# Kernel tuning notes

Hardware: AMD Instinct MI355X
Metric: run time of the kernel (lower is better)

The kernel has to match this reference:

```python
import jax, jax.numpy as jnp
import numpy as np
from jax import lax

OBS_LEN = 8
PRED_LEN = 12
BATCH = 131072
EMB = 128
HID = 128


def _lstm_cell(h, c, x, Wih, Whh, b):
    # PyTorch LSTM gate order: i, f, g, o
    z = x @ Wih + h @ Whh + b  # (B, 4H)
    i, f, g, o = jnp.split(z, 4, axis=-1)
    c_new = jax.nn.sigmoid(f) * c + jax.nn.sigmoid(i) * jnp.tanh(g)
    h_new = jax.nn.sigmoid(o) * jnp.tanh(c_new)
    return h_new, c_new


def setup_inputs() -> dict:
    key = jax.random.key(0)
    ks = jax.random.split(key, 8)
    p = lambda k, s: jax.random.normal(k, s, dtype=jnp.float32) * 0.1
    return {
        "obs_traj": jax.random.normal(ks[0], (OBS_LEN, BATCH, 2), dtype=jnp.float32),
        # encoder input embedding (Linear 2 -> EMB)
        "We": p(ks[1], (2, EMB)), "be": jnp.zeros((EMB,), jnp.float32),
        # encoder LSTM
        "Wih_e": p(ks[2], (EMB, 4 * HID)), "Whh_e": p(ks[3], (HID, 4 * HID)),
        "b_e": jnp.zeros((4 * HID,), jnp.float32),
        # decoder input embedding (Linear 2 -> EMB)
        "Wd": p(ks[4], (2, EMB)), "bd": jnp.zeros((EMB,), jnp.float32),
        # decoder LSTM
        "Wih_d": p(ks[5], (EMB, 4 * HID)), "Whh_d": p(ks[6], (HID, 4 * HID)),
        "b_d": jnp.zeros((4 * HID,), jnp.float32),
        # hidden2pos (Linear HID -> 2)
        "Wo": p(ks[7], (HID, 2)), "bo": jnp.zeros((2,), jnp.float32),
        "pred_len": PRED_LEN,
    }


def reference(obs_traj, We, be, Wih_e, Whh_e, b_e, Wd, bd, Wih_d, Whh_d, b_d, Wo, bo, pred_len):
    B = obs_traj.shape[1]
    H = Whh_e.shape[0]
    dt = obs_traj.dtype

    # ---- Encoder: embed positions, run LSTM over obs_len ----
    emb = obs_traj @ We + be  # (obs_len, B, EMB)
    h0 = jnp.zeros((B, H), dt)
    c0 = jnp.zeros((B, H), dt)

    def enc_step(carry, x_t):
        h, c = carry
        h, c = _lstm_cell(h, c, x_t, Wih_e, Whh_e, b_e)
        return (h, c), None

    (h_enc, _), _ = lax.scan(enc_step, (h0, c0), emb)

    # ---- Decoder: state = (h_final, zeros); first pos directly from h_final ----
    pos0 = h_enc @ Wo + bo  # (B, 2)
    h_d = h_enc
    c_d = jnp.zeros_like(h_enc)

    def dec_step(carry, _):
        h, c, pos = carry
        x = pos @ Wd + bd  # embed previous predicted position
        h, c = _lstm_cell(h, c, x, Wih_d, Whh_d, b_d)
        pos_new = h @ Wo + bo
        return (h, c, pos_new), pos_new

    _, rest = lax.scan(dec_step, (h_d, c_d, pos0), None, length=pred_len - 1)
    pred_traj = jnp.concatenate([pos0[None], rest], axis=0)  # (pred_len, B, 2)
    return pred_traj
```

## Files before the change

### kernel.cpp

```cpp
#include <hip/hip_runtime.h>


#define OBS_LEN 8
#define PRED_LEN 12
#define BATCH 131072
#define HID 128
#define NZ 512
#define KWT 128
#define XK 32
#define A2S 40

typedef float f32x4 __attribute__((ext_vector_type(4)));
typedef float f32x2 __attribute__((ext_vector_type(2)));
typedef unsigned short u16x8 __attribute__((ext_vector_type(8)));
typedef __bf16 bf16x8 __attribute__((ext_vector_type(8)));

#define K2F 1.4426950408889634f

static __device__ __forceinline__ unsigned short cvt1(float f) {
  __bf16 b = (__bf16)f;
  return __builtin_bit_cast(unsigned short, b);
}
static __device__ __forceinline__ float bf2f(unsigned short h) {
  return __uint_as_float(((unsigned int)h) << 16);
}

__global__ void prep_weights(const float* __restrict__ We,   const float* __restrict__ be,
                             const float* __restrict__ Wih_e,const float* __restrict__ Whh_e,
                             const float* __restrict__ b_e,
                             const float* __restrict__ Wd,   const float* __restrict__ bd,
                             const float* __restrict__ Wih_d,const float* __restrict__ Whh_d,
                             const float* __restrict__ b_d,
                             const float* __restrict__ Wo,   const float* __restrict__ bo,
                             unsigned short* __restrict__ wt_enc,
                             unsigned short* __restrict__ wt_dec,
                             unsigned short* __restrict__ xw_enc,
                             float* __restrict__ auxf_dec) {
  const int c = blockIdx.x & (NZ - 1);
  const bool dec = blockIdx.x >= NZ;
  const int cg = c >> 6, gate = (c >> 4) & 3, cl = c & 15;
  const int unit = cg * 16 + cl;
  const int n = gate * HID + unit;
  const float s = (gate == 2) ? (-2.f * K2F) : (-K2F);

  const float* Whh = dec ? Whh_d : Whh_e;
  const float* Wih = dec ? Wih_d : Wih_e;
  const float* Wem = dec ? Wd : We;
  const float* bem = dec ? bd : be;
  const float* bl  = dec ? b_d : b_e;
  unsigned short* wt = dec ? wt_dec : wt_enc;

  float wx = 0.f, wy = 0.f;
  for (int e = 0; e < HID; ++e) {
    wx += Wem[e] * Wih[e * NZ + n];
    wy += Wem[HID + e] * Wih[e * NZ + n];
  }
  for (int k = threadIdx.x; k < KWT; k += 64) {
    float v = Whh[k * NZ + n];
    if (dec) v += Wo[k * 2] * wx + Wo[k * 2 + 1] * wy;
    wt[c * KWT + k] = cvt1(s * v);
  }
  if (threadIdx.x == 0) {
    float bb = bl[n];
    for (int e = 0; e < HID; ++e) bb += bem[e] * Wih[e * NZ + n];
    if (dec) {
      bb += bo[0] * wx + bo[1] * wy;
      auxf_dec[c] = s * bb;
    } else {
      unsigned short* xr = xw_enc + c * XK;
      for (int k = 5; k < XK; ++k) xr[k] = 0;
      xr[0] = cvt1(s * wx); xr[1] = cvt1(s * wy); xr[2] = cvt1(s * bb);
      xr[3] = xr[0]; xr[4] = xr[1];
    }
  }
}


#define MFMA(A, B, C)                                                          \
  __builtin_amdgcn_mfma_f32_16x16x32_bf16(                                     \
      __builtin_bit_cast(bf16x8, (A)), __builtin_bit_cast(bf16x8, (B)), (C),   \
      0, 0, 0)

#define EXP4(D, S)                                                             \
  { f32x4 _s = (S);                                                            \
    D[0] = __builtin_amdgcn_exp2f(_s[0]); D[1] = __builtin_amdgcn_exp2f(_s[1]);\
    D[2] = __builtin_amdgcn_exp2f(_s[2]); D[3] = __builtin_amdgcn_exp2f(_s[3]); }
#define RCP4(D, S)                                                             \
  { f32x4 _r = (S);                                                            \
    D[0] = __builtin_amdgcn_rcpf(_r[0]); D[1] = __builtin_amdgcn_rcpf(_r[1]);  \
    D[2] = __builtin_amdgcn_rcpf(_r[2]); D[3] = __builtin_amdgcn_rcpf(_r[3]); }

#define LOADW_BF(WT)                                                           \
  { _Pragma("unroll")                                                          \
    for (int kc = 0; kc < 4; ++kc) {                                           \
      _Pragma("unroll")                                                        \
      for (int g = 0; g < 4; ++g)                                              \
        bfr[kc][g] =                                                           \
            *(const u16x8*)&(WT)[(cg * 64 + g * 16 + l15) * KWT + kc * 32 +    \
                                 l4 * 8];                                      \
    } }

#define MMH(ACC, X)                                                            \
  { _Pragma("unroll")                                                          \
    for (int kc = 0; kc < 4; ++kc) {                                           \
      const int mm_g = (((kc * 4 + l4) ^ l15) << 3);                           \
      u16x8 mm_a0 = *(const u16x8*)&hL[(X)*4096 + l15 * 128 + mm_g];           \
      u16x8 mm_a1 = *(const u16x8*)&hL[(X)*4096 + (16 + l15) * 128 + mm_g];    \
      _Pragma("unroll")                                                        \
      for (int g = 0; g < 4; ++g) {                                            \
        ACC[0][g] = MFMA(mm_a0, bfr[kc][g], ACC[0][g]);                        \
        ACC[1][g] = MFMA(mm_a1, bfr[kc][g], ACC[1][g]);                        \
      } } }

#define MMXE(ACC, X)                                                           \
  { u16x8 mm_a2a = *(const u16x8*)&A2[(X)*32 * A2S + l15 * A2S + l4 * 8];      \
    u16x8 mm_a2b =                                                             \
        *(const u16x8*)&A2[(X)*32 * A2S + (16 + l15) * A2S + l4 * 8];          \
    _Pragma("unroll")                                                          \
    for (int g = 0; g < 4; ++g) {                                              \
      ACC[0][g] = MFMA(mm_a2a, xfr[g], ZROV);                                  \
      ACC[1][g] = MFMA(mm_a2b, xfr[g], ZROV);                                  \
    }                                                                          \
    MMH(ACC, X) }

#define INITD(ACC)                                                             \
  { _Pragma("unroll")                                                          \
    for (int m = 0; m < 2; ++m) {                                              \
      _Pragma("unroll")                                                        \
      for (int g = 0; g < 4; ++g)                                              \
        ACC[m][g] = (f32x4){bbD[g], bbD[g], bbD[g], bbD[g]};                   \
    } }

#define GATEC(ACC, CRR, X)                                                     \
  { _Pragma("unroll")                                                          \
    for (int m = 0; m < 2; ++m) {                                              \
      f32x4 g_eB, g_eA, g_eG, g_eO;                                            \
      EXP4(g_eB, ACC[m][0]) EXP4(g_eA, ACC[m][1])                              \
      EXP4(g_eG, ACC[m][2]) EXP4(g_eO, ACC[m][3])                              \
      f32x4 g_a1 = 1.f + g_eA, g_b1 = 1.f + g_eB, g_g1 = 1.f + g_eG;           \
      f32x4 g_bg = g_b1 * g_g1;                                                \
      f32x4 g_rd; RCP4(g_rd, g_a1 * g_bg)                                      \
      f32x4 g_cv = (CRR[m] * g_bg + (1.f - g_eG) * g_a1) * g_rd;               \
      CRR[m] = g_cv;                                                           \
      f32x4 g_eC; EXP4(g_eC, g_cv * (-2.f * K2F))                              \
      f32x4 g_rh; RCP4(g_rh, (1.f + g_eO) * (1.f + g_eC))                      \
      f32x4 g_hv = (1.f - g_eC) * g_rh;                                        \
      const int g_R0 = 16 * m + l4 * 4;                                        \
      _Pragma("unroll")                                                        \
      for (int r = 0; r < 4; ++r)                                              \
        hL[(X)*4096 + (g_R0 + r) * 128 +                                       \
           ((uh ^ ((g_R0 + r) & 15)) << 3) + ul] = cvt1(g_hv[r]);              \
    } }

#define POSC(S, X)                                                             \
  { const int pp_r = tid >> 4;                                                 \
    u16x8 pp_h = *(const u16x8*)&hL[(X)*4096 + pp_r * 128 +                    \
                                    ((pq ^ (pp_r & 15)) << 3)];                \
    f32x2 pp_s = (f32x2){0.f, 0.f};                                            \
    pp_s += bf2f(pp_h[0]) * (f32x2){wo0[0], wo0[1]};                           \
    pp_s += bf2f(pp_h[1]) * (f32x2){wo0[2], wo0[3]};                           \
    pp_s += bf2f(pp_h[2]) * (f32x2){wo1[0], wo1[1]};                           \
    pp_s += bf2f(pp_h[3]) * (f32x2){wo1[2], wo1[3]};                           \
    pp_s += bf2f(pp_h[4]) * (f32x2){wo2[0], wo2[1]};                           \
    pp_s += bf2f(pp_h[5]) * (f32x2){wo2[2], wo2[3]};                           \
    pp_s += bf2f(pp_h[6]) * (f32x2){wo3[0], wo3[1]};                           \
    pp_s += bf2f(pp_h[7]) * (f32x2){wo3[2], wo3[3]};                           \
    pp_s[0] += __shfl_xor(pp_s[0], 1); pp_s[1] += __shfl_xor(pp_s[1], 1);      \
    pp_s[0] += __shfl_xor(pp_s[0], 2); pp_s[1] += __shfl_xor(pp_s[1], 2);      \
    pp_s[0] += __shfl_xor(pp_s[0], 4); pp_s[1] += __shfl_xor(pp_s[1], 4);      \
    pp_s[0] += __shfl_xor(pp_s[0], 8); pp_s[1] += __shfl_xor(pp_s[1], 8);      \
    if (pq == 0) {                                                             \
      float2 pp_o; pp_o.x = pp_s[0] + bo0; pp_o.y = pp_s[1] + bo1;             \
      ((float2*)out)[(size_t)(S)*BATCH + row0 + (X)*32 + pp_r] = pp_o;         \
    } }

#define STAGE_OBS_A2(T, X)                                                     \
  if (tid < 32) {                                                              \
    float2 so_p =                                                              \
        ((const float2*)obs)[(size_t)(T)*BATCH + row0 + (X)*32 + tid];         \
    unsigned short so_x = cvt1(so_p.x), so_y = cvt1(so_p.y);                   \
    unsigned short* so_r = &A2[(X)*32 * A2S + tid * A2S];                      \
    so_r[0] = so_x; so_r[1] = so_y; so_r[2] = 0x3F80u;                         \
    so_r[3] = cvt1(so_p.x - bf2f(so_x));                                       \
    so_r[4] = cvt1(so_p.y - bf2f(so_y));                                       \
  }

__global__ __launch_bounds__(512, 2) void lstm_fused(
    const float* __restrict__ obs,
    const unsigned short* __restrict__ wt_enc,
    const unsigned short* __restrict__ wt_dec,
    const unsigned short* __restrict__ xw_enc,
    const float* __restrict__ auxf_dec,
    const float* __restrict__ Wo, const float* __restrict__ bo,
    float* __restrict__ out) {
  __shared__ unsigned short hL[2 * 32 * 128];
  __shared__ unsigned short A2[2 * 32 * A2S];

  const int tid = threadIdx.x;
  const int lane = tid & 63;
  const int cg = tid >> 6;
  const int l15 = lane & 15;
  const int l4 = lane >> 4;
  const int pq = tid & 15;
  const int row0 = blockIdx.x * 64;
  const int u = cg * 16 + l15, uh = u >> 3, ul = u & 7;
  const float bo0 = bo[0], bo1 = bo[1];
  const f32x4 ZROV = {0.f, 0.f, 0.f, 0.f};

  {
    u16x8 z8 = (u16x8){0, 0, 0, 0, 0, 0, 0, 0};
    *(u16x8*)&hL[tid * 8] = z8;
    *(u16x8*)&hL[4096 + tid * 8] = z8;
    unsigned short* az = &A2[tid * 5];
    az[0] = 0; az[1] = 0; az[2] = 0; az[3] = 0; az[4] = 0;
  }
  const float* wop = Wo + pq * 16;
  const f32x4 wo0 = *(const f32x4*)wop;
  const f32x4 wo1 = *(const f32x4*)(wop + 4);
  const f32x4 wo2 = *(const f32x4*)(wop + 8);
  const f32x4 wo3 = *(const f32x4*)(wop + 12);

  u16x8 bfr[4][4], xfr[4];
  LOADW_BF(wt_enc);
#pragma unroll
  for (int g = 0; g < 4; ++g)
    xfr[g] = *(const u16x8*)&xw_enc[(cg * 64 + g * 16 + l15) * XK + l4 * 8];

  f32x4 accA[2][4], accB[2][4];
  f32x4 crrA[2], crrB[2];
  crrA[0] = crrA[1] = ZROV;
  crrB[0] = crrB[1] = ZROV;
  __syncthreads();

  STAGE_OBS_A2(0, 0)
  __syncthreads();

#pragma unroll 1
  for (int t = 0; t < OBS_LEN; ++t) {
    if (t > 0) { GATEC(accB, crrB, 1) }
    STAGE_OBS_A2(t, 1)
    MMXE(accA, 0)
    __syncthreads();
    GATEC(accA, crrA, 0)
    if (t + 1 < OBS_LEN) { STAGE_OBS_A2(t + 1, 0) }
    MMXE(accB, 1)
    __syncthreads();
  }

  LOADW_BF(wt_dec);
  float bbD[4];
#pragma unroll
  for (int g = 0; g < 4; ++g) bbD[g] = auxf_dec[cg * 64 + g * 16 + l15];
  crrA[0] = crrA[1] = ZROV;

  GATEC(accB, crrB, 1)
  POSC(0, 0)
  INITD(accA)
  MMH(accA, 0)
  __syncthreads();
  crrB[0] = crrB[1] = ZROV;

  GATEC(accA, crrA, 0)
  POSC(0, 1)
  INITD(accB)
  MMH(accB, 1)
  __syncthreads();

#pragma unroll 1
  for (int d = 2; d < PRED_LEN; ++d) {
    GATEC(accB, crrB, 1)
    POSC(d - 1, 0)
    INITD(accA)
    MMH(accA, 0)
    __syncthreads();
    GATEC(accA, crrA, 0)
    POSC(d - 1, 1)
    INITD(accB)
    MMH(accB, 1)
    __syncthreads();
  }

  GATEC(accB, crrB, 1)
  POSC(PRED_LEN - 1, 0)
  __syncthreads();
  POSC(PRED_LEN - 1, 1)
}

extern "C" void kernel_launch(void* const* d_in, const int* in_sizes, int n_in,
                              void* d_out, int out_size, void* d_ws, size_t ws_size,
                              hipStream_t stream) {
  const float* obs   = (const float*)d_in[0];
  const float* We    = (const float*)d_in[1];
  const float* be    = (const float*)d_in[2];
  const float* Wih_e = (const float*)d_in[3];
  const float* Whh_e = (const float*)d_in[4];
  const float* b_e   = (const float*)d_in[5];
  const float* Wd    = (const float*)d_in[6];
  const float* bd    = (const float*)d_in[7];
  const float* Wih_d = (const float*)d_in[8];
  const float* Whh_d = (const float*)d_in[9];
  const float* b_d   = (const float*)d_in[10];
  const float* Wo    = (const float*)d_in[11];
  const float* bo    = (const float*)d_in[12];
  float* out = (float*)d_out;

  unsigned short* wt_enc = (unsigned short*)d_ws;
  unsigned short* wt_dec = wt_enc + NZ * KWT;
  unsigned short* xw_enc = wt_dec + NZ * KWT;
  float* auxf_dec = (float*)(xw_enc + NZ * XK);

  hipLaunchKernelGGL(prep_weights, dim3(2 * NZ), dim3(64), 0, stream,
                     We, be, Wih_e, Whh_e, b_e, Wd, bd, Wih_d, Whh_d, b_d,
                     Wo, bo, wt_enc, wt_dec, xw_enc, auxf_dec);
  hipLaunchKernelGGL(lstm_fused, dim3(BATCH / 64), dim3(512), 0, stream,
                     obs, wt_enc, wt_dec, xw_enc, auxf_dec, Wo, bo, out);
}
```

Measured before the change: 502.2 us.

## Double-buffer LSTM hidden state to halve barriers per timestep

Ping-pong buffers for the hidden state in LDS and for the staged observation inputs let both 32-row halves run their matmuls, then both gate updates, with a single barrier per timestep instead of two. The old schedule staggered the two halves to overlap gate math with MFMA. The new one groups all MFMAs and then all gate math inside each step. The decoder bias is also folded into the first MFMA's accumulator input instead of being set with separate initialisation. LDS use doubles, which may limit occupancy, and the interleaving of the two halves across barriers is lost.

```diff
diff --git a/kernel.cpp b/kernel.cpp
--- a/kernel.cpp
+++ b/kernel.cpp
@@ -9,6 +9,7 @@
 #define KWT 128
 #define XK 32
 #define A2S 40
+#define A2Q (2 * 32 * A2S)
 
 typedef float f32x4 __attribute__((ext_vector_type(4)));
 typedef float f32x2 __attribute__((ext_vector_type(2)));
@@ -100,38 +101,54 @@
                                  l4 * 8];                                      \
     } }
 
-#define MMH(ACC, X)                                                            \
+#define MMH(ACC, X, P)                                                         \
   { _Pragma("unroll")                                                          \
     for (int kc = 0; kc < 4; ++kc) {                                           \
       const int mm_g = (((kc * 4 + l4) ^ l15) << 3);                           \
-      u16x8 mm_a0 = *(const u16x8*)&hL[(X)*4096 + l15 * 128 + mm_g];           \
-      u16x8 mm_a1 = *(const u16x8*)&hL[(X)*4096 + (16 + l15) * 128 + mm_g];    \
+      const int mb = (X)*8192 + (P)*4096;                                      \
+      u16x8 mm_a0 = *(const u16x8*)&hL[mb + l15 * 128 + mm_g];                 \
+      u16x8 mm_a1 = *(const u16x8*)&hL[mb + (16 + l15) * 128 + mm_g];          \
       _Pragma("unroll")                                                        \
       for (int g = 0; g < 4; ++g) {                                            \
         ACC[0][g] = MFMA(mm_a0, bfr[kc][g], ACC[0][g]);                        \
         ACC[1][g] = MFMA(mm_a1, bfr[kc][g], ACC[1][g]);                        \
       } } }
 
-#define MMXE(ACC, X)                                                           \
-  { u16x8 mm_a2a = *(const u16x8*)&A2[(X)*32 * A2S + l15 * A2S + l4 * 8];      \
+#define MMXE(ACC, X, P, Q)                                                     \
+  { u16x8 mm_a2a =                                                             \
+        *(const u16x8*)&A2[(Q)*A2Q + ((X)*32 + l15) * A2S + l4 * 8];           \
     u16x8 mm_a2b =                                                             \
-        *(const u16x8*)&A2[(X)*32 * A2S + (16 + l15) * A2S + l4 * 8];          \
+        *(const u16x8*)&A2[(Q)*A2Q + ((X)*32 + 16 + l15) * A2S + l4 * 8];      \
     _Pragma("unroll")                                                          \
     for (int g = 0; g < 4; ++g) {                                              \
       ACC[0][g] = MFMA(mm_a2a, xfr[g], ZROV);                                  \
       ACC[1][g] = MFMA(mm_a2b, xfr[g], ZROV);                                  \
     }                                                                          \
-    MMH(ACC, X) }
-
-#define INITD(ACC)                                                             \
-  { _Pragma("unroll")                                                          \
-    for (int m = 0; m < 2; ++m) {                                              \
-      _Pragma("unroll")                                                        \
-      for (int g = 0; g < 4; ++g)                                              \
-        ACC[m][g] = (f32x4){bbD[g], bbD[g], bbD[g], bbD[g]};                   \
-    } }
-
-#define GATEC(ACC, CRR, X)                                                     \
+    MMH(ACC, X, P) }
+
+#define MMHD(ACC, X, P)                                                        \
+  { { const int mm_g = ((l4 ^ l15) << 3);                                      \
+      const int mb = (X)*8192 + (P)*4096;                                      \
+      u16x8 mm_a0 = *(const u16x8*)&hL[mb + l15 * 128 + mm_g];                 \
+      u16x8 mm_a1 = *(const u16x8*)&hL[mb + (16 + l15) * 128 + mm_g];          \
+      _Pragma("unroll")                                                        \
+      for (int g = 0; g < 4; ++g) {                                            \
+        ACC[0][g] = MFMA(mm_a0, bfr[0][g], bbV[g]);                            \
+        ACC[1][g] = MFMA(mm_a1, bfr[0][g], bbV[g]);                            \
+      } }                                                                      \
+    _Pragma("unroll")                                                          \
+    for (int kc = 1; kc < 4; ++kc) {                                           \
+      const int mm_g = (((kc * 4 + l4) ^ l15) << 3);                           \
+      const int mb = (X)*8192 + (P)*4096;                                      \
+      u16x8 mm_a0 = *(const u16x8*)&hL[mb + l15 * 128 + mm_g];                 \
+      u16x8 mm_a1 = *(const u16x8*)&hL[mb + (16 + l15) * 128 + mm_g];          \
+      _Pragma("unroll")                                                        \
+      for (int g = 0; g < 4; ++g) {                                            \
+        ACC[0][g] = MFMA(mm_a0, bfr[kc][g], ACC[0][g]);                        \
+        ACC[1][g] = MFMA(mm_a1, bfr[kc][g], ACC[1][g]);                        \
+      } } }
+
+#define GATEC(ACC, CRR, X, P)                                                  \
   { _Pragma("unroll")                                                          \
     for (int m = 0; m < 2; ++m) {                                              \
       f32x4 g_eB, g_eA, g_eG, g_eO;                                            \
@@ -148,13 +165,13 @@
       const int g_R0 = 16 * m + l4 * 4;                                        \
       _Pragma("unroll")                                                        \
       for (int r = 0; r < 4; ++r)                                              \
-        hL[(X)*4096 + (g_R0 + r) * 128 +                                       \
+        hL[(X)*8192 + (P)*4096 + (g_R0 + r) * 128 +                            \
            ((uh ^ ((g_R0 + r) & 15)) << 3) + ul] = cvt1(g_hv[r]);              \
     } }
 
-#define POSC(S, X)                                                             \
+#define POSC(S, X, P)                                                          \
   { const int pp_r = tid >> 4;                                                 \
-    u16x8 pp_h = *(const u16x8*)&hL[(X)*4096 + pp_r * 128 +                    \
+    u16x8 pp_h = *(const u16x8*)&hL[(X)*8192 + (P)*4096 + pp_r * 128 +         \
                                     ((pq ^ (pp_r & 15)) << 3)];                \
     f32x2 pp_s = (f32x2){0.f, 0.f};                                            \
     pp_s += bf2f(pp_h[0]) * (f32x2){wo0[0], wo0[1]};                           \
@@ -174,12 +191,11 @@
       ((float2*)out)[(size_t)(S)*BATCH + row0 + (X)*32 + pp_r] = pp_o;         \
     } }
 
-#define STAGE_OBS_A2(T, X)                                                     \
-  if (tid < 32) {                                                              \
-    float2 so_p =                                                              \
-        ((const float2*)obs)[(size_t)(T)*BATCH + row0 + (X)*32 + tid];         \
+#define STAGE_A2(T, Q)                                                         \
+  if (tid < 64) {                                                              \
+    float2 so_p = ((const float2*)obs)[(size_t)(T)*BATCH + row0 + tid];        \
     unsigned short so_x = cvt1(so_p.x), so_y = cvt1(so_p.y);                   \
-    unsigned short* so_r = &A2[(X)*32 * A2S + tid * A2S];                      \
+    unsigned short* so_r = &A2[(Q)*A2Q + tid * A2S];                           \
     so_r[0] = so_x; so_r[1] = so_y; so_r[2] = 0x3F80u;                         \
     so_r[3] = cvt1(so_p.x - bf2f(so_x));                                       \
     so_r[4] = cvt1(so_p.y - bf2f(so_y));                                       \
@@ -193,8 +209,8 @@
     const float* __restrict__ auxf_dec,
     const float* __restrict__ Wo, const float* __restrict__ bo,
     float* __restrict__ out) {
-  __shared__ unsigned short hL[2 * 32 * 128];
-  __shared__ unsigned short A2[2 * 32 * A2S];
+  __shared__ unsigned short hL[2 * 2 * 32 * 128];
+  __shared__ unsigned short A2[2 * A2Q];
 
   const int tid = threadIdx.x;
   const int lane = tid & 63;
@@ -210,9 +226,10 @@
   {
     u16x8 z8 = (u16x8){0, 0, 0, 0, 0, 0, 0, 0};
     *(u16x8*)&hL[tid * 8] = z8;
-    *(u16x8*)&hL[4096 + tid * 8] = z8;
-    unsigned short* az = &A2[tid * 5];
+    *(u16x8*)&hL[8192 + tid * 8] = z8;
+    unsigned short* az = &A2[tid * 10];
     az[0] = 0; az[1] = 0; az[2] = 0; az[3] = 0; az[4] = 0;
+    az[5] = 0; az[6] = 0; az[7] = 0; az[8] = 0; az[9] = 0;
   }
   const float* wop = Wo + pq * 16;
   const f32x4 wo0 = *(const f32x4*)wop;
@@ -232,58 +249,44 @@
   crrB[0] = crrB[1] = ZROV;
   __syncthreads();
 
-  STAGE_OBS_A2(0, 0)
+  STAGE_A2(0, 0)
   __syncthreads();
 
 #pragma unroll 1
   for (int t = 0; t < OBS_LEN; ++t) {
-    if (t > 0) { GATEC(accB, crrB, 1) }
-    STAGE_OBS_A2(t, 1)
-    MMXE(accA, 0)
+    const int p = t & 1;
+    if (t + 1 < OBS_LEN) { STAGE_A2(t + 1, p ^ 1) }
+    MMXE(accA, 0, p, p)
+    MMXE(accB, 1, p, p)
+    GATEC(accA, crrA, 0, p ^ 1)
+    GATEC(accB, crrB, 1, p ^ 1)
     __syncthreads();
-    GATEC(accA, crrA, 0)
-    if (t + 1 < OBS_LEN) { STAGE_OBS_A2(t + 1, 0) }
-    MMXE(accB, 1)
+  }
+
+  LOADW_BF(wt_dec);
+  f32x4 bbV[4];
+#pragma unroll
+  for (int g = 0; g < 4; ++g) {
+    float b_ = auxf_dec[cg * 64 + g * 16 + l15];
+    bbV[g] = (f32x4){b_, b_, b_, b_};
+  }
+  crrA[0] = crrA[1] = ZROV;
+  crrB[0] = crrB[1] = ZROV;
+
+#pragma unroll 1
+  for (int d = 1; d < PRED_LEN; ++d) {
+    const int p = (d - 1) & 1;
+    MMHD(accA, 0, p)
+    MMHD(accB, 1, p)
+    POSC(d - 1, 0, p)
+    POSC(d - 1, 1, p)
+    GATEC(accA, crrA, 0, p ^ 1)
+    GATEC(accB, crrB, 1, p ^ 1)
     __syncthreads();
   }
 
-  LOADW_BF(wt_dec);
-  float bbD[4];
-#pragma unroll
-  for (int g = 0; g < 4; ++g) bbD[g] = auxf_dec[cg * 64 + g * 16 + l15];
-  crrA[0] = crrA[1] = ZROV;
-
-  GATEC(accB, crrB, 1)
-  POSC(0, 0)
-  INITD(accA)
-  MMH(accA, 0)
-  __syncthreads();
-  crrB[0] = crrB[1] = ZROV;
-
-  GATEC(accA, crrA, 0)
-  POSC(0, 1)
-  INITD(accB)
-  MMH(accB, 1)
-  __syncthreads();
-
-#pragma unroll 1
-  for (int d = 2; d < PRED_LEN; ++d) {
-    GATEC(accB, crrB, 1)
-    POSC(d - 1, 0)
-    INITD(accA)
-    MMH(accA, 0)
-    __syncthreads();
-    GATEC(accA, crrA, 0)
-    POSC(d - 1, 1)
-    INITD(accB)
-    MMH(accB, 1)
-    __syncthreads();
-  }
-
-  GATEC(accB, crrB, 1)
-  POSC(PRED_LEN - 1, 0)
-  __syncthreads();
-  POSC(PRED_LEN - 1, 1)
+  POSC(PRED_LEN - 1, 0, 1)
+  POSC(PRED_LEN - 1, 1, 1)
 }
 
 extern "C" void kernel_launch(void* const* d_in, const int* in_sizes, int n_in,
```

Result: no change. 501.0 us (-0.2%).

## Stage LSTM weights in LDS and use 1024-thread blocks with single-phase steps

Applied to the files above, without the earlier changes.

Moves the recurrent weight matrix out of per-thread registers into about 154 KB of dynamic shared memory, staged once for the encoder and once for the decoder. Each block now runs 16 waves over 64 rows, split as two row groups by eight column groups. The earlier ping-pong between two 32-row halves, which overlapped gate math with MFMA work, is replaced by a simple matmul, sync, gate, sync sequence. The input-projection padding shrinks from 32 to 8 columns, and output weights are reloaded inside the position step instead of held in registers. The aim is to free the VGPRs that held weights, at the cost of an LDS read for every MFMA B-fragment, only one block per CU, and less overlap between compute phases.

```diff
diff --git a/kernel.cpp b/kernel.cpp
--- a/kernel.cpp
+++ b/kernel.cpp
@@ -7,8 +7,6 @@
 #define HID 128
 #define NZ 512
 #define KWT 128
-#define XK 32
-#define A2S 40
 
 typedef float f32x4 __attribute__((ext_vector_type(4)));
 typedef float f32x2 __attribute__((ext_vector_type(2)));
@@ -67,10 +65,10 @@
       bb += bo[0] * wx + bo[1] * wy;
       auxf_dec[c] = s * bb;
     } else {
-      unsigned short* xr = xw_enc + c * XK;
-      for (int k = 5; k < XK; ++k) xr[k] = 0;
+      unsigned short* xr = xw_enc + c * 8;
       xr[0] = cvt1(s * wx); xr[1] = cvt1(s * wy); xr[2] = cvt1(s * bb);
       xr[3] = xr[0]; xr[4] = xr[1];
+      xr[5] = 0; xr[6] = 0; xr[7] = 0;
     }
   }
 }
@@ -90,102 +88,116 @@
     D[0] = __builtin_amdgcn_rcpf(_r[0]); D[1] = __builtin_amdgcn_rcpf(_r[1]);  \
     D[2] = __builtin_amdgcn_rcpf(_r[2]); D[3] = __builtin_amdgcn_rcpf(_r[3]); }
 
-#define LOADW_BF(WT)                                                           \
+#define STAGE_WT(SRC)                                                          \
+  { const int sw_c = tid >> 1, sw_h = (tid & 1) * 8;                           \
+    const unsigned short* sw_s = (SRC) + sw_c * KWT + sw_h * 8;                \
+    unsigned short* sw_d = Wl + sw_c * KWT;                                    \
+    _Pragma("unroll")                                                          \
+    for (int j = 0; j < 8; ++j)                                                \
+      *(u16x8*)&sw_d[((sw_h + j) ^ (sw_c & 15)) << 3] =                        \
+          *(const u16x8*)(sw_s + j * 8);                                       \
+  }
+
+#define MMH()                                                                  \
   { _Pragma("unroll")                                                          \
     for (int kc = 0; kc < 4; ++kc) {                                           \
-      _Pragma("unroll")                                                        \
-      for (int g = 0; g < 4; ++g)                                              \
-        bfr[kc][g] =                                                           \
-            *(const u16x8*)&(WT)[(cg * 64 + g * 16 + l15) * KWT + kc * 32 +    \
-                                 l4 * 8];                                      \
-    } }
-
-#define MMH(ACC, X)                                                            \
-  { _Pragma("unroll")                                                          \
-    for (int kc = 0; kc < 4; ++kc) {                                           \
-      const int mm_g = (((kc * 4 + l4) ^ l15) << 3);                           \
-      u16x8 mm_a0 = *(const u16x8*)&hL[(X)*4096 + l15 * 128 + mm_g];           \
-      u16x8 mm_a1 = *(const u16x8*)&hL[(X)*4096 + (16 + l15) * 128 + mm_g];    \
+      const int sl = (((kc * 4 + l4) ^ l15) << 3);                            \
+      u16x8 a0 = *(const u16x8*)&hL[(rbase + l15) * 128 + sl];                 \
+      u16x8 a1 = *(const u16x8*)&hL[(rbase + 16 + l15) * 128 + sl];            \
       _Pragma("unroll")                                                        \
       for (int g = 0; g < 4; ++g) {                                            \
-        ACC[0][g] = MFMA(mm_a0, bfr[kc][g], ACC[0][g]);                        \
-        ACC[1][g] = MFMA(mm_a1, bfr[kc][g], ACC[1][g]);                        \
+        u16x8 bf = *(const u16x8*)&Wl[(cg * 64 + g * 16 + l15) * 128 + sl];    \
+        acc[0][g] = MFMA(a0, bf, acc[0][g]);                                   \
+        acc[1][g] = MFMA(a1, bf, acc[1][g]);                                   \
       } } }
 
-#define MMXE(ACC, X)                                                           \
-  { u16x8 mm_a2a = *(const u16x8*)&A2[(X)*32 * A2S + l15 * A2S + l4 * 8];      \
-    u16x8 mm_a2b =                                                             \
-        *(const u16x8*)&A2[(X)*32 * A2S + (16 + l15) * A2S + l4 * 8];          \
-    _Pragma("unroll")                                                          \
-    for (int g = 0; g < 4; ++g) {                                              \
-      ACC[0][g] = MFMA(mm_a2a, xfr[g], ZROV);                                  \
-      ACC[1][g] = MFMA(mm_a2b, xfr[g], ZROV);                                  \
+#define MMXE(Q)                                                                \
+  { u16x8 za = (u16x8){0, 0, 0, 0, 0, 0, 0, 0};                                \
+    u16x8 a2a = za, a2b = za, xf0 = za, xf1 = za, xf2 = za, xf3 = za;          \
+    if (l4 == 0) {                                                             \
+      a2a = *(const u16x8*)&A2[(Q)*512 + (rbase + l15) * 8];                   \
+      a2b = *(const u16x8*)&A2[(Q)*512 + (rbase + 16 + l15) * 8];              \
+      xf0 = *(const u16x8*)&xwL[(cg * 64 + l15) * 8];                          \
+      xf1 = *(const u16x8*)&xwL[(cg * 64 + 16 + l15) * 8];                     \
+      xf2 = *(const u16x8*)&xwL[(cg * 64 + 32 + l15) * 8];                     \
+      xf3 = *(const u16x8*)&xwL[(cg * 64 + 48 + l15) * 8];                     \
     }                                                                          \
-    MMH(ACC, X) }
-
-#define INITD(ACC)                                                             \
+    acc[0][0] = MFMA(a2a, xf0, ZROV); acc[1][0] = MFMA(a2b, xf0, ZROV);        \
+    acc[0][1] = MFMA(a2a, xf1, ZROV); acc[1][1] = MFMA(a2b, xf1, ZROV);        \
+    acc[0][2] = MFMA(a2a, xf2, ZROV); acc[1][2] = MFMA(a2b, xf2, ZROV);        \
+    acc[0][3] = MFMA(a2a, xf3, ZROV); acc[1][3] = MFMA(a2b, xf3, ZROV);        \
+    MMH() }
+
+#define INITD()                                                                \
   { _Pragma("unroll")                                                          \
     for (int m = 0; m < 2; ++m) {                                              \
       _Pragma("unroll")                                                        \
       for (int g = 0; g < 4; ++g)                                              \
-        ACC[m][g] = (f32x4){bbD[g], bbD[g], bbD[g], bbD[g]};                   \
+        acc[m][g] = (f32x4){bbD[g], bbD[g], bbD[g], bbD[g]};                   \
     } }
 
-#define GATEC(ACC, CRR, X)                                                     \
+#define GATEC()                                                                \
   { _Pragma("unroll")                                                          \
     for (int m = 0; m < 2; ++m) {                                              \
       f32x4 g_eB, g_eA, g_eG, g_eO;                                            \
-      EXP4(g_eB, ACC[m][0]) EXP4(g_eA, ACC[m][1])                              \
-      EXP4(g_eG, ACC[m][2]) EXP4(g_eO, ACC[m][3])                              \
+      EXP4(g_eB, acc[m][0]) EXP4(g_eA, acc[m][1])                              \
+      EXP4(g_eG, acc[m][2]) EXP4(g_eO, acc[m][3])                              \
       f32x4 g_a1 = 1.f + g_eA, g_b1 = 1.f + g_eB, g_g1 = 1.f + g_eG;           \
       f32x4 g_bg = g_b1 * g_g1;                                                \
       f32x4 g_rd; RCP4(g_rd, g_a1 * g_bg)                                      \
-      f32x4 g_cv = (CRR[m] * g_bg + (1.f - g_eG) * g_a1) * g_rd;               \
-      CRR[m] = g_cv;                                                           \
+      f32x4 g_cv = (crr[m] * g_bg + (1.f - g_eG) * g_a1) * g_rd;               \
+      crr[m] = g_cv;                                                           \
       f32x4 g_eC; EXP4(g_eC, g_cv * (-2.f * K2F))                              \
       f32x4 g_rh; RCP4(g_rh, (1.f + g_eO) * (1.f + g_eC))                      \
       f32x4 g_hv = (1.f - g_eC) * g_rh;                                        \
-      const int g_R0 = 16 * m + l4 * 4;                                        \
+      const int g_R0 = rbase + 16 * m + l4 * 4;                                \
       _Pragma("unroll")                                                        \
       for (int r = 0; r < 4; ++r)                                              \
-        hL[(X)*4096 + (g_R0 + r) * 128 +                                       \
-           ((uh ^ ((g_R0 + r) & 15)) << 3) + ul] = cvt1(g_hv[r]);              \
+        hL[(g_R0 + r) * 128 + ((uh ^ ((g_R0 + r) & 15)) << 3) + ul] =          \
+            cvt1(g_hv[r]);                                                     \
     } }
 
-#define POSC(S, X)                                                             \
+#define POSC(S)                                                                \
   { const int pp_r = tid >> 4;                                                 \
-    u16x8 pp_h = *(const u16x8*)&hL[(X)*4096 + pp_r * 128 +                    \
-                                    ((pq ^ (pp_r & 15)) << 3)];                \
+    u16x8 pp_h =                                                               \
+        *(const u16x8*)&hL[pp_r * 128 + ((pq ^ (pp_r & 15)) << 3)];            \
+    const float* pp_w = Wo + pq * 16;                                          \
+    f32x4 pw0 = *(const f32x4*)pp_w;                                           \
+    f32x4 pw1 = *(const f32x4*)(pp_w + 4);                                     \
+    f32x4 pw2 = *(const f32x4*)(pp_w + 8);                                     \
+    f32x4 pw3 = *(const f32x4*)(pp_w + 12);                                    \
     f32x2 pp_s = (f32x2){0.f, 0.f};                                            \
-    pp_s += bf2f(pp_h[0]) * (f32x2){wo0[0], wo0[1]};                           \
-    pp_s += bf2f(pp_h[1]) * (f32x2){wo0[2], wo0[3]};                           \
-    pp_s += bf2f(pp_h[2]) * (f32x2){wo1[0], wo1[1]};                           \
-    pp_s += bf2f(pp_h[3]) * (f32x2){wo1[2], wo1[3]};                           \
-    pp_s += bf2f(pp_h[4]) * (f32x2){wo2[0], wo2[1]};                           \
-    pp_s += bf2f(pp_h[5]) * (f32x2){wo2[2], wo2[3]};                           \
-    pp_s += bf2f(pp_h[6]) * (f32x2){wo3[0], wo3[1]};                           \
-    pp_s += bf2f(pp_h[7]) * (f32x2){wo3[2], wo3[3]};                           \
+    pp_s += bf2f(pp_h[0]) * (f32x2){pw0[0], pw0[1]};                           \
+    pp_s += bf2f(pp_h[1]) * (f32x2){pw0[2], pw0[3]};                           \
+    pp_s += bf2f(pp_h[2]) * (f32x2){pw1[0], pw1[1]};                           \
+    pp_s += bf2f(pp_h[3]) * (f32x2){pw1[2], pw1[3]};                           \
+    pp_s += bf2f(pp_h[4]) * (f32x2){pw2[0], pw2[1]};                           \
+    pp_s += bf2f(pp_h[5]) * (f32x2){pw2[2], pw2[3]};                           \
+    pp_s += bf2f(pp_h[6]) * (f32x2){pw3[0], pw3[1]};                           \
+    pp_s += bf2f(pp_h[7]) * (f32x2){pw3[2], pw3[3]};                           \
     pp_s[0] += __shfl_xor(pp_s[0], 1); pp_s[1] += __shfl_xor(pp_s[1], 1);      \
     pp_s[0] += __shfl_xor(pp_s[0], 2); pp_s[1] += __shfl_xor(pp_s[1], 2);      \
     pp_s[0] += __shfl_xor(pp_s[0], 4); pp_s[1] += __shfl_xor(pp_s[1], 4);      \
     pp_s[0] += __shfl_xor(pp_s[0], 8); pp_s[1] += __shfl_xor(pp_s[1], 8);      \
     if (pq == 0) {                                                             \
       float2 pp_o; pp_o.x = pp_s[0] + bo0; pp_o.y = pp_s[1] + bo1;             \
-      ((float2*)out)[(size_t)(S)*BATCH + row0 + (X)*32 + pp_r] = pp_o;         \
+      ((float2*)out)[(size_t)(S)*BATCH + row0 + pp_r] = pp_o;                  \
     } }
 
-#define STAGE_OBS_A2(T, X)                                                     \
-  if (tid < 32) {                                                              \
-    float2 so_p =                                                              \
-        ((const float2*)obs)[(size_t)(T)*BATCH + row0 + (X)*32 + tid];         \
+#define STAGE_A2(T, Q)                                                         \
+  if (tid < 64) {                                                              \
+    float2 so_p = ((const float2*)obs)[(size_t)(T)*BATCH + row0 + tid];        \
     unsigned short so_x = cvt1(so_p.x), so_y = cvt1(so_p.y);                   \
-    unsigned short* so_r = &A2[(X)*32 * A2S + tid * A2S];                      \
+    unsigned short* so_r = &A2[(Q)*512 + tid * 8];                             \
     so_r[0] = so_x; so_r[1] = so_y; so_r[2] = 0x3F80u;                         \
     so_r[3] = cvt1(so_p.x - bf2f(so_x));                                       \
     so_r[4] = cvt1(so_p.y - bf2f(so_y));                                       \
-  }
-
-__global__ __launch_bounds__(512, 2) void lstm_fused(
+    so_r[5] = 0; so_r[6] = 0; so_r[7] = 0;                                     \
+  }
+
+#define SMEM_BYTES ((NZ * KWT + 64 * 128 + NZ * 8 + 2 * 64 * 8) * 2)
+
+__global__ __launch_bounds__(1024, 4) void lstm_fused(
     const float* __restrict__ obs,
     const unsigned short* __restrict__ wt_enc,
     const unsigned short* __restrict__ wt_dec,
@@ -193,12 +205,17 @@
     const float* __restrict__ auxf_dec,
     const float* __restrict__ Wo, const float* __restrict__ bo,
     float* __restrict__ out) {
-  __shared__ unsigned short hL[2 * 32 * 128];
-  __shared__ unsigned short A2[2 * 32 * A2S];
+  extern __shared__ unsigned short sm[];
+  unsigned short* Wl  = sm;
+  unsigned short* hL  = sm + NZ * KWT;
+  unsigned short* xwL = hL + 64 * 128;
+  unsigned short* A2  = xwL + NZ * 8;
 
   const int tid = threadIdx.x;
   const int lane = tid & 63;
-  const int cg = tid >> 6;
+  const int wv = tid >> 6;
+  const int rg = wv >> 3, cg = wv & 7;
+  const int rbase = rg * 32;
   const int l15 = lane & 15;
   const int l4 = lane >> 4;
   const int pq = tid & 15;
@@ -207,83 +224,47 @@
   const float bo0 = bo[0], bo1 = bo[1];
   const f32x4 ZROV = {0.f, 0.f, 0.f, 0.f};
 
+  STAGE_WT(wt_enc)
+  if (tid < NZ) *(u16x8*)&xwL[tid * 8] = *(const u16x8*)&xw_enc[tid * 8];
   {
     u16x8 z8 = (u16x8){0, 0, 0, 0, 0, 0, 0, 0};
     *(u16x8*)&hL[tid * 8] = z8;
-    *(u16x8*)&hL[4096 + tid * 8] = z8;
-    unsigned short* az = &A2[tid * 5];
-    az[0] = 0; az[1] = 0; az[2] = 0; az[3] = 0; az[4] = 0;
-  }
-  const float* wop = Wo + pq * 16;
-  const f32x4 wo0 = *(const f32x4*)wop;
-  const f32x4 wo1 = *(const f32x4*)(wop + 4);
-  const f32x4 wo2 = *(const f32x4*)(wop + 8);
-  const f32x4 wo3 = *(const f32x4*)(wop + 12);
-
-  u16x8 bfr[4][4], xfr[4];
-  LOADW_BF(wt_enc);
-#pragma unroll
-  for (int g = 0; g < 4; ++g)
-    xfr[g] = *(const u16x8*)&xw_enc[(cg * 64 + g * 16 + l15) * XK + l4 * 8];
-
-  f32x4 accA[2][4], accB[2][4];
-  f32x4 crrA[2], crrB[2];
-  crrA[0] = crrA[1] = ZROV;
-  crrB[0] = crrB[1] = ZROV;
-  __syncthreads();
-
-  STAGE_OBS_A2(0, 0)
+    if (tid < 128) *(u16x8*)&A2[tid * 8] = z8;
+  }
+  STAGE_A2(0, 0)
+
+  f32x4 acc[2][4];
+  f32x4 crr[2];
+  crr[0] = crr[1] = ZROV;
   __syncthreads();
 
 #pragma unroll 1
   for (int t = 0; t < OBS_LEN; ++t) {
-    if (t > 0) { GATEC(accB, crrB, 1) }
-    STAGE_OBS_A2(t, 1)
-    MMXE(accA, 0)
+    const int q = t & 1;
+    MMXE(q)
     __syncthreads();
-    GATEC(accA, crrA, 0)
-    if (t + 1 < OBS_LEN) { STAGE_OBS_A2(t + 1, 0) }
-    MMXE(accB, 1)
+    GATEC()
+    if (t + 1 < OBS_LEN) { STAGE_A2(t + 1, q ^ 1) }
     __syncthreads();
   }
 
-  LOADW_BF(wt_dec);
+  STAGE_WT(wt_dec)
   float bbD[4];
 #pragma unroll
   for (int g = 0; g < 4; ++g) bbD[g] = auxf_dec[cg * 64 + g * 16 + l15];
-  crrA[0] = crrA[1] = ZROV;
-
-  GATEC(accB, crrB, 1)
-  POSC(0, 0)
-  INITD(accA)
-  MMH(accA, 0)
+  crr[0] = crr[1] = ZROV;
   __syncthreads();
-  crrB[0] = crrB[1] = ZROV;
-
-  GATEC(accA, crrA, 0)
-  POSC(0, 1)
-  INITD(accB)
-  MMH(accB, 1)
-  __syncthreads();
 
 #pragma unroll 1
-  for (int d = 2; d < PRED_LEN; ++d) {
-    GATEC(accB, crrB, 1)
-    POSC(d - 1, 0)
-    INITD(accA)
-    MMH(accA, 0)
+  for (int d = 1; d < PRED_LEN; ++d) {
+    INITD()
+    MMH()
+    POSC(d - 1)
     __syncthreads();
-    GATEC(accA, crrA, 0)
-    POSC(d - 1, 1)
-    INITD(accB)
-    MMH(accB, 1)
+    GATEC()
     __syncthreads();
   }
-
-  GATEC(accB, crrB, 1)
-  POSC(PRED_LEN - 1, 0)
-  __syncthreads();
-  POSC(PRED_LEN - 1, 1)
+  POSC(PRED_LEN - 1)
 }
 
 extern "C" void kernel_launch(void* const* d_in, const int* in_sizes, int n_in,
@@ -307,11 +288,15 @@
   unsigned short* wt_enc = (unsigned short*)d_ws;
   unsigned short* wt_dec = wt_enc + NZ * KWT;
   unsigned short* xw_enc = wt_dec + NZ * KWT;
-  float* auxf_dec = (float*)(xw_enc + NZ * XK);
+  float* auxf_dec = (float*)(xw_enc + NZ * 8);
+
+  hipFuncSetAttribute((const void*)lstm_fused,
+                      hipFuncAttributeMaxDynamicSharedMemorySize, SMEM_BYTES);
 
   hipLaunchKernelGGL(prep_weights, dim3(2 * NZ), dim3(64), 0, stream,
                      We, be, Wih_e, Whh_e, b_e, Wd, bd, Wih_d, Whh_d, b_d,
                      Wo, bo, wt_enc, wt_dec, xw_enc, auxf_dec);
-  hipLaunchKernelGGL(lstm_fused, dim3(BATCH / 64), dim3(512), 0, stream,
-                     obs, wt_enc, wt_dec, xw_enc, auxf_dec, Wo, bo, out);
-}
+  hipLaunchKernelGGL(lstm_fused, dim3(BATCH / 64), dim3(1024), SMEM_BYTES,
+                     stream, obs, wt_enc, wt_dec, xw_enc, auxf_dec, Wo, bo,
+                     out);
+}
```

New measurement: 505.5 us. Within noise of the previous version (+0.7%).

## Split LSTM gates across 16 waves with transposed MFMA gate-interleaved layout

Applied to the files above, without the earlier changes.

Moves the fused LSTM kernel from 512 to 1024 threads per block. Each wave now owns 8 hidden units and all four of their gates, with the weight rows permuted so one MFMA output register holds i,f,g,o for a single unit. The matmul is transposed (weights as A, hidden state as B) and the gate math is done per scalar, which shrinks per-thread register arrays and the bias init is folded into the first MFMA. This raises wave-level parallelism and lowers register pressure per thread. The cost is more waves contending at each barrier, and the launch_bounds change may force register spilling.

```diff
diff --git a/kernel.cpp b/kernel.cpp
--- a/kernel.cpp
+++ b/kernel.cpp
@@ -8,11 +8,11 @@
 #define NZ 512
 #define KWT 128
 #define XK 32
-#define A2S 40
 
 typedef float f32x4 __attribute__((ext_vector_type(4)));
 typedef float f32x2 __attribute__((ext_vector_type(2)));
 typedef unsigned short u16x8 __attribute__((ext_vector_type(8)));
+typedef unsigned short u16x4 __attribute__((ext_vector_type(4)));
 typedef __bf16 bf16x8 __attribute__((ext_vector_type(8)));
 
 #define K2F 1.4426950408889634f
@@ -38,8 +38,8 @@
                              float* __restrict__ auxf_dec) {
   const int c = blockIdx.x & (NZ - 1);
   const bool dec = blockIdx.x >= NZ;
-  const int cg = c >> 6, gate = (c >> 4) & 3, cl = c & 15;
-  const int unit = cg * 16 + cl;
+  const int w = c >> 5, ct = (c >> 4) & 1, q = (c >> 2) & 3, gate = c & 3;
+  const int unit = w * 8 + ct * 4 + q;
   const int n = gate * HID + unit;
   const float s = (gate == 2) ? (-2.f * K2F) : (-K2F);
 
@@ -81,95 +81,79 @@
       __builtin_bit_cast(bf16x8, (A)), __builtin_bit_cast(bf16x8, (B)), (C),   \
       0, 0, 0)
 
-#define EXP4(D, S)                                                             \
-  { f32x4 _s = (S);                                                            \
-    D[0] = __builtin_amdgcn_exp2f(_s[0]); D[1] = __builtin_amdgcn_exp2f(_s[1]);\
-    D[2] = __builtin_amdgcn_exp2f(_s[2]); D[3] = __builtin_amdgcn_exp2f(_s[3]); }
-#define RCP4(D, S)                                                             \
-  { f32x4 _r = (S);                                                            \
-    D[0] = __builtin_amdgcn_rcpf(_r[0]); D[1] = __builtin_amdgcn_rcpf(_r[1]);  \
-    D[2] = __builtin_amdgcn_rcpf(_r[2]); D[3] = __builtin_amdgcn_rcpf(_r[3]); }
-
-#define LOADW_BF(WT)                                                           \
-  { _Pragma("unroll")                                                          \
+#define HB(X, RT, KC)                                                          \
+  (*(const u16x8*)&hL[(X)*4096 + ((RT)*16 + l15) * 128 +                       \
+                      ((((KC)*4 + l4) ^ l15) << 3)])
+#define A2B(X, RT)                                                             \
+  (*(const u16x8*)&A2[(X)*1024 + ((RT)*16 + l15) * 32 + l4 * 8])
+
+#define MMXE(ACC, X)                                                           \
+  { u16x8 mm_b0 = A2B(X, 0), mm_b1 = A2B(X, 1);                                \
+    _Pragma("unroll")                                                          \
+    for (int ct = 0; ct < 2; ++ct) {                                           \
+      ACC[0][ct] = MFMA(xfr[ct], mm_b0, ZROV);                                 \
+      ACC[1][ct] = MFMA(xfr[ct], mm_b1, ZROV);                                 \
+    }                                                                          \
+    _Pragma("unroll")                                                          \
     for (int kc = 0; kc < 4; ++kc) {                                           \
+      u16x8 mm_h0 = HB(X, 0, kc), mm_h1 = HB(X, 1, kc);                        \
       _Pragma("unroll")                                                        \
-      for (int g = 0; g < 4; ++g)                                              \
-        bfr[kc][g] =                                                           \
-            *(const u16x8*)&(WT)[(cg * 64 + g * 16 + l15) * KWT + kc * 32 +    \
-                                 l4 * 8];                                      \
-    } }
-
-#define MMH(ACC, X)                                                            \
-  { _Pragma("unroll")                                                          \
-    for (int kc = 0; kc < 4; ++kc) {                                           \
-      const int mm_g = (((kc * 4 + l4) ^ l15) << 3);                           \
-      u16x8 mm_a0 = *(const u16x8*)&hL[(X)*4096 + l15 * 128 + mm_g];           \
-      u16x8 mm_a1 = *(const u16x8*)&hL[(X)*4096 + (16 + l15) * 128 + mm_g];    \
+      for (int ct = 0; ct < 2; ++ct) {                                         \
+        ACC[0][ct] = MFMA(bfr[ct][kc], mm_h0, ACC[0][ct]);                     \
+        ACC[1][ct] = MFMA(bfr[ct][kc], mm_h1, ACC[1][ct]);                     \
+      } } }
+
+#define MMHD(ACC, X)                                                           \
+  { { u16x8 mm_h0 = HB(X, 0, 0), mm_h1 = HB(X, 1, 0);                          \
       _Pragma("unroll")                                                        \
-      for (int g = 0; g < 4; ++g) {                                            \
-        ACC[0][g] = MFMA(mm_a0, bfr[kc][g], ACC[0][g]);                        \
-        ACC[1][g] = MFMA(mm_a1, bfr[kc][g], ACC[1][g]);                        \
+      for (int ct = 0; ct < 2; ++ct) {                                         \
+        ACC[0][ct] = MFMA(bfr[ct][0], mm_h0, bbV[ct]);                         \
+        ACC[1][ct] = MFMA(bfr[ct][0], mm_h1, bbV[ct]);                         \
+      } }                                                                      \
+    _Pragma("unroll")                                                          \
+    for (int kc = 1; kc < 4; ++kc) {                                           \
+      u16x8 mm_h0 = HB(X, 0, kc), mm_h1 = HB(X, 1, kc);                        \
+      _Pragma("unroll")                                                        \
+      for (int ct = 0; ct < 2; ++ct) {                                         \
+        ACC[0][ct] = MFMA(bfr[ct][kc], mm_h0, ACC[0][ct]);                     \
+        ACC[1][ct] = MFMA(bfr[ct][kc], mm_h1, ACC[1][ct]);                     \
       } } }
 
-#define MMXE(ACC, X)                                                           \
-  { u16x8 mm_a2a = *(const u16x8*)&A2[(X)*32 * A2S + l15 * A2S + l4 * 8];      \
-    u16x8 mm_a2b =                                                             \
-        *(const u16x8*)&A2[(X)*32 * A2S + (16 + l15) * A2S + l4 * 8];          \
-    _Pragma("unroll")                                                          \
-    for (int g = 0; g < 4; ++g) {                                              \
-      ACC[0][g] = MFMA(mm_a2a, xfr[g], ZROV);                                  \
-      ACC[1][g] = MFMA(mm_a2b, xfr[g], ZROV);                                  \
-    }                                                                          \
-    MMH(ACC, X) }
-
-#define INITD(ACC)                                                             \
-  { _Pragma("unroll")                                                          \
-    for (int m = 0; m < 2; ++m) {                                              \
-      _Pragma("unroll")                                                        \
-      for (int g = 0; g < 4; ++g)                                              \
-        ACC[m][g] = (f32x4){bbD[g], bbD[g], bbD[g], bbD[g]};                   \
-    } }
-
-#define GATEC(ACC, CRR, X)                                                     \
-  { _Pragma("unroll")                                                          \
-    for (int m = 0; m < 2; ++m) {                                              \
-      f32x4 g_eB, g_eA, g_eG, g_eO;                                            \
-      EXP4(g_eB, ACC[m][0]) EXP4(g_eA, ACC[m][1])                              \
-      EXP4(g_eG, ACC[m][2]) EXP4(g_eO, ACC[m][3])                              \
-      f32x4 g_a1 = 1.f + g_eA, g_b1 = 1.f + g_eB, g_g1 = 1.f + g_eG;           \
-      f32x4 g_bg = g_b1 * g_g1;                                                \
-      f32x4 g_rd; RCP4(g_rd, g_a1 * g_bg)                                      \
-      f32x4 g_cv = (CRR[m] * g_bg + (1.f - g_eG) * g_a1) * g_rd;               \
-      CRR[m] = g_cv;                                                           \
-      f32x4 g_eC; EXP4(g_eC, g_cv * (-2.f * K2F))                              \
-      f32x4 g_rh; RCP4(g_rh, (1.f + g_eO) * (1.f + g_eC))                      \
-      f32x4 g_hv = (1.f - g_eC) * g_rh;                                        \
-      const int g_R0 = 16 * m + l4 * 4;                                        \
-      _Pragma("unroll")                                                        \
-      for (int r = 0; r < 4; ++r)                                              \
-        hL[(X)*4096 + (g_R0 + r) * 128 +                                       \
-           ((uh ^ ((g_R0 + r) & 15)) << 3) + ul] = cvt1(g_hv[r]);              \
-    } }
+#define GATEQ(ACC, CRR, X, RT, CT)                                             \
+  { float g_eB = __builtin_amdgcn_exp2f(ACC[RT][CT][0]);                       \
+    float g_eA = __builtin_amdgcn_exp2f(ACC[RT][CT][1]);                       \
+    float g_eG = __builtin_amdgcn_exp2f(ACC[RT][CT][2]);                       \
+    float g_eO = __builtin_amdgcn_exp2f(ACC[RT][CT][3]);                       \
+    float g_a1 = 1.f + g_eA, g_b1 = 1.f + g_eB, g_g1 = 1.f + g_eG;             \
+    float g_bg = g_b1 * g_g1;                                                  \
+    float g_rd = __builtin_amdgcn_rcpf(g_a1 * g_bg);                           \
+    float g_cv = (CRR[(RT)*2 + (CT)] * g_bg + (1.f - g_eG) * g_a1) * g_rd;     \
+    CRR[(RT)*2 + (CT)] = g_cv;                                                 \
+    float g_eC = __builtin_amdgcn_exp2f(-2.f * K2F * g_cv);                    \
+    float g_rh = __builtin_amdgcn_rcpf((1.f + g_eO) * (1.f + g_eC));           \
+    float g_hv = (1.f - g_eC) * g_rh;                                          \
+    hL[(X)*4096 + ((RT)*16 + l15) * 128 + ((wv ^ l15) << 3) + (CT)*4 + l4] =   \
+        cvt1(g_hv);                                                            \
+  }
 
 #define POSC(S, X)                                                             \
-  { const int pp_r = tid >> 4;                                                 \
-    u16x8 pp_h = *(const u16x8*)&hL[(X)*4096 + pp_r * 128 +                    \
-                                    ((pq ^ (pp_r & 15)) << 3)];                \
+  { const int pp_r = tid >> 5, pp_q = tid & 31;                                \
+    u16x4 pp_h = *(const u16x4*)&hL[(X)*4096 + pp_r * 128 +                    \
+                                    (((pp_q >> 1) ^ (pp_r & 15)) << 3) +       \
+                                    (pp_q & 1) * 4];                           \
+    f32x4 pp_w0 = *(const f32x4*)&WoL[pp_q * 8];                               \
+    f32x4 pp_w1 = *(const f32x4*)&WoL[pp_q * 8 + 4];                           \
     f32x2 pp_s = (f32x2){0.f, 0.f};                                            \
-    pp_s += bf2f(pp_h[0]) * (f32x2){wo0[0], wo0[1]};                           \
-    pp_s += bf2f(pp_h[1]) * (f32x2){wo0[2], wo0[3]};                           \
-    pp_s += bf2f(pp_h[2]) * (f32x2){wo1[0], wo1[1]};                           \
-    pp_s += bf2f(pp_h[3]) * (f32x2){wo1[2], wo1[3]};                           \
-    pp_s += bf2f(pp_h[4]) * (f32x2){wo2[0], wo2[1]};                           \
-    pp_s += bf2f(pp_h[5]) * (f32x2){wo2[2], wo2[3]};                           \
-    pp_s += bf2f(pp_h[6]) * (f32x2){wo3[0], wo3[1]};                           \
-    pp_s += bf2f(pp_h[7]) * (f32x2){wo3[2], wo3[3]};                           \
-    pp_s[0] += __shfl_xor(pp_s[0], 1); pp_s[1] += __shfl_xor(pp_s[1], 1);      \
-    pp_s[0] += __shfl_xor(pp_s[0], 2); pp_s[1] += __shfl_xor(pp_s[1], 2);      \
-    pp_s[0] += __shfl_xor(pp_s[0], 4); pp_s[1] += __shfl_xor(pp_s[1], 4);      \
-    pp_s[0] += __shfl_xor(pp_s[0], 8); pp_s[1] += __shfl_xor(pp_s[1], 8);      \
-    if (pq == 0) {                                                             \
+    pp_s += bf2f(pp_h[0]) * (f32x2){pp_w0[0], pp_w0[1]};                       \
+    pp_s += bf2f(pp_h[1]) * (f32x2){pp_w0[2], pp_w0[3]};                       \
+    pp_s += bf2f(pp_h[2]) * (f32x2){pp_w1[0], pp_w1[1]};                       \
+    pp_s += bf2f(pp_h[3]) * (f32x2){pp_w1[2], pp_w1[3]};                       \
+    pp_s[0] += __shfl_xor(pp_s[0], 1);  pp_s[1] += __shfl_xor(pp_s[1], 1);     \
+    pp_s[0] += __shfl_xor(pp_s[0], 2);  pp_s[1] += __shfl_xor(pp_s[1], 2);     \
+    pp_s[0] += __shfl_xor(pp_s[0], 4);  pp_s[1] += __shfl_xor(pp_s[1], 4);     \
+    pp_s[0] += __shfl_xor(pp_s[0], 8);  pp_s[1] += __shfl_xor(pp_s[1], 8);     \
+    pp_s[0] += __shfl_xor(pp_s[0], 16); pp_s[1] += __shfl_xor(pp_s[1], 16);    \
+    if (pp_q == 0) {                                                           \
       float2 pp_o; pp_o.x = pp_s[0] + bo0; pp_o.y = pp_s[1] + bo1;             \
       ((float2*)out)[(size_t)(S)*BATCH + row0 + (X)*32 + pp_r] = pp_o;         \
     } }
@@ -179,13 +163,13 @@
     float2 so_p =                                                              \
         ((const float2*)obs)[(size_t)(T)*BATCH + row0 + (X)*32 + tid];         \
     unsigned short so_x = cvt1(so_p.x), so_y = cvt1(so_p.y);                   \
-    unsigned short* so_r = &A2[(X)*32 * A2S + tid * A2S];                      \
+    unsigned short* so_r = &A2[(X)*1024 + tid * 32];                           \
     so_r[0] = so_x; so_r[1] = so_y; so_r[2] = 0x3F80u;                         \
     so_r[3] = cvt1(so_p.x - bf2f(so_x));                                       \
     so_r[4] = cvt1(so_p.y - bf2f(so_y));                                       \
   }
 
-__global__ __launch_bounds__(512, 2) void lstm_fused(
+__global__ __launch_bounds__(1024, 4) void lstm_fused(
     const float* __restrict__ obs,
     const unsigned short* __restrict__ wt_enc,
     const unsigned short* __restrict__ wt_dec,
@@ -194,42 +178,44 @@
     const float* __restrict__ Wo, const float* __restrict__ bo,
     float* __restrict__ out) {
   __shared__ unsigned short hL[2 * 32 * 128];
-  __shared__ unsigned short A2[2 * 32 * A2S];
+  __shared__ unsigned short A2[2 * 32 * 32];
+  __shared__ float WoL[HID * 2];
 
   const int tid = threadIdx.x;
   const int lane = tid & 63;
-  const int cg = tid >> 6;
+  const int wv = tid >> 6;
   const int l15 = lane & 15;
   const int l4 = lane >> 4;
-  const int pq = tid & 15;
   const int row0 = blockIdx.x * 64;
-  const int u = cg * 16 + l15, uh = u >> 3, ul = u & 7;
   const float bo0 = bo[0], bo1 = bo[1];
   const f32x4 ZROV = {0.f, 0.f, 0.f, 0.f};
 
   {
     u16x8 z8 = (u16x8){0, 0, 0, 0, 0, 0, 0, 0};
     *(u16x8*)&hL[tid * 8] = z8;
-    *(u16x8*)&hL[4096 + tid * 8] = z8;
-    unsigned short* az = &A2[tid * 5];
-    az[0] = 0; az[1] = 0; az[2] = 0; az[3] = 0; az[4] = 0;
-  }
-  const float* wop = Wo + pq * 16;
-  const f32x4 wo0 = *(const f32x4*)wop;
-  const f32x4 wo1 = *(const f32x4*)(wop + 4);
-  const f32x4 wo2 = *(const f32x4*)(wop + 8);
-  const f32x4 wo3 = *(const f32x4*)(wop + 12);
-
-  u16x8 bfr[4][4], xfr[4];
-  LOADW_BF(wt_enc);
-#pragma unroll
-  for (int g = 0; g < 4; ++g)
-    xfr[g] = *(const u16x8*)&xw_enc[(cg * 64 + g * 16 + l15) * XK + l4 * 8];
-
-  f32x4 accA[2][4], accB[2][4];
-  f32x4 crrA[2], crrB[2];
-  crrA[0] = crrA[1] = ZROV;
-  crrB[0] = crrB[1] = ZROV;
+    if (tid < 256) *(u16x8*)&A2[tid * 8] = z8;
+    if (tid < HID) {
+      WoL[tid * 2] = Wo[tid * 2];
+      WoL[tid * 2 + 1] = Wo[tid * 2 + 1];
+    }
+  }
+
+  u16x8 bfr[2][4];
+  u16x8 xfr[2];
+#pragma unroll
+  for (int ct = 0; ct < 2; ++ct) {
+#pragma unroll
+    for (int kc = 0; kc < 4; ++kc)
+      bfr[ct][kc] = *(const u16x8*)&wt_enc[(wv * 32 + ct * 16 + l15) * KWT +
+                                           kc * 32 + l4 * 8];
+    xfr[ct] = *(const u16x8*)&xw_enc[(wv * 32 + ct * 16 + l15) * XK + l4 * 8];
+  }
+
+  f32x4 accA[2][2], accB[2][2];
+  float crrA[4], crrB[4];
+#pragma unroll
+  for (int i = 0; i < 4; ++i) { crrA[i] = 0.f; crrB[i] = 0.f; }
+  f32x4 bbV[2];
   __syncthreads();
 
   STAGE_OBS_A2(0, 0)
@@ -237,50 +223,61 @@
 
 #pragma unroll 1
   for (int t = 0; t < OBS_LEN; ++t) {
-    if (t > 0) { GATEC(accB, crrB, 1) }
+    if (t > 0) {
+      GATEQ(accB, crrB, 1, 0, 0) GATEQ(accB, crrB, 1, 0, 1)
+      GATEQ(accB, crrB, 1, 1, 0) GATEQ(accB, crrB, 1, 1, 1)
+    }
     STAGE_OBS_A2(t, 1)
     MMXE(accA, 0)
     __syncthreads();
-    GATEC(accA, crrA, 0)
+    GATEQ(accA, crrA, 0, 0, 0) GATEQ(accA, crrA, 0, 0, 1)
+    GATEQ(accA, crrA, 0, 1, 0) GATEQ(accA, crrA, 0, 1, 1)
     if (t + 1 < OBS_LEN) { STAGE_OBS_A2(t + 1, 0) }
     MMXE(accB, 1)
     __syncthreads();
   }
 
-  LOADW_BF(wt_dec);
-  float bbD[4];
-#pragma unroll
-  for (int g = 0; g < 4; ++g) bbD[g] = auxf_dec[cg * 64 + g * 16 + l15];
-  crrA[0] = crrA[1] = ZROV;
-
-  GATEC(accB, crrB, 1)
+#pragma unroll
+  for (int ct = 0; ct < 2; ++ct) {
+#pragma unroll
+    for (int kc = 0; kc < 4; ++kc)
+      bfr[ct][kc] = *(const u16x8*)&wt_dec[(wv * 32 + ct * 16 + l15) * KWT +
+                                           kc * 32 + l4 * 8];
+    bbV[ct] = *(const f32x4*)&auxf_dec[wv * 32 + ct * 16 + l4 * 4];
+  }
+#pragma unroll
+  for (int i = 0; i < 4; ++i) crrA[i] = 0.f;
+
+  GATEQ(accB, crrB, 1, 0, 0) GATEQ(accB, crrB, 1, 0, 1)
+  GATEQ(accB, crrB, 1, 1, 0) GATEQ(accB, crrB, 1, 1, 1)
+  MMHD(accA, 0)
   POSC(0, 0)
-  INITD(accA)
-  MMH(accA, 0)
-  __syncthreads();
-  crrB[0] = crrB[1] = ZROV;
-
-  GATEC(accA, crrA, 0)
+  __syncthreads();
+#pragma unroll
+  for (int i = 0; i < 4; ++i) crrB[i] = 0.f;
+
+  GATEQ(accA, crrA, 0, 0, 0) GATEQ(accA, crrA, 0, 0, 1)
+  GATEQ(accA, crrA, 0, 1, 0) GATEQ(accA, crrA, 0, 1, 1)
+  MMHD(accB, 1)
   POSC(0, 1)
-  INITD(accB)
-  MMH(accB, 1)
   __syncthreads();
 
 #pragma unroll 1
   for (int d = 2; d < PRED_LEN; ++d) {
-    GATEC(accB, crrB, 1)
+    GATEQ(accB, crrB, 1, 0, 0) GATEQ(accB, crrB, 1, 0, 1)
+    GATEQ(accB, crrB, 1, 1, 0) GATEQ(accB, crrB, 1, 1, 1)
+    MMHD(accA, 0)
     POSC(d - 1, 0)
-    INITD(accA)
-    MMH(accA, 0)
     __syncthreads();
-    GATEC(accA, crrA, 0)
+    GATEQ(accA, crrA, 0, 0, 0) GATEQ(accA, crrA, 0, 0, 1)
+    GATEQ(accA, crrA, 0, 1, 0) GATEQ(accA, crrA, 0, 1, 1)
+    MMHD(accB, 1)
     POSC(d - 1, 1)
-    INITD(accB)
-    MMH(accB, 1)
     __syncthreads();
   }
 
-  GATEC(accB, crrB, 1)
+  GATEQ(accB, crrB, 1, 0, 0) GATEQ(accB, crrB, 1, 0, 1)
+  GATEQ(accB, crrB, 1, 1, 0) GATEQ(accB, crrB, 1, 1, 1)
   POSC(PRED_LEN - 1, 0)
   __syncthreads();
   POSC(PRED_LEN - 1, 1)
@@ -312,6 +309,6 @@
   hipLaunchKernelGGL(prep_weights, dim3(2 * NZ), dim3(64), 0, stream,
                      We, be, Wih_e, Whh_e, b_e, Wd, bd, Wih_d, Whh_d, b_d,
                      Wo, bo, wt_enc, wt_dec, xw_enc, auxf_dec);
-  hipLaunchKernelGGL(lstm_fused, dim3(BATCH / 64), dim3(512), 0, stream,
+  hipLaunchKernelGGL(lstm_fused, dim3(BATCH / 64), dim3(1024), 0, stream,
                      obs, wt_enc, wt_dec, xw_enc, auxf_dec, Wo, bo, out);
 }
```

Result: no change. 508.9 us (+1.4%).
